# Kernel optimization log

Measured on AMD Instinct MI355X. Metric: run time of the kernel, lower is better.

The kernel has to match this reference:

```python
import jax, jax.numpy as jnp
import numpy as np


def setup_inputs() -> dict:
    key = jax.random.key(0)
    ks = jax.random.split(key, 7)
    B, EN, DE, E, U, T = 8, 512, 64, 512, 512, 100  # batch, max_words, max_label, emb, units, topics
    return {
        "en_seq": jax.random.normal(ks[0], (B, EN, E), dtype=jnp.float32),
        "de_seq": jax.random.normal(ks[1], (B, DE, E), dtype=jnp.float32),
        "topics": jax.random.uniform(ks[2], (B, T), dtype=jnp.float32),
        "w_en": jax.random.normal(ks[3], (E, U), dtype=jnp.float32) * 0.05,
        "w_de": jax.random.normal(ks[4], (E, U), dtype=jnp.float32) * 0.05,
        "nu": jax.random.normal(ks[5], (U,), dtype=jnp.float32) * 0.05,
        "wt": jax.random.normal(ks[6], (E, T), dtype=jnp.float32) * 0.05,
    }


def reference(en_seq, de_seq, topics, w_en, w_de, nu, wt):
    # Additive (Bahdanau-style) attention with a per-batch topic bias.
    att_en = jnp.einsum("bie,eu->biu", en_seq, w_en)        # [B, EN, U]
    att_de = jnp.einsum("bje,eu->bju", de_seq, w_de)        # [B, DE, U]
    topics_w = jnp.einsum("bt,ut->bu", topics, wt)          # [B, U] (wt is [E,U-dim? no: E==U])
    # co_m[b, j, i, u] = att_en[b,i,u] + att_de[b,j,u] + topics_w[b,u]
    co_m = jnp.tanh(att_en[:, None, :, :] + att_de[:, :, None, :]
                    + topics_w[:, None, None, :])           # [B, DE, EN, U]
    mu = jnp.einsum("bjiu,u->bji", co_m, nu)                # [B, DE, EN]
    alphas = jax.nn.softmax(mu, axis=-1)                    # softmax over encoder positions
    p_gen = jax.nn.sigmoid(mu)
    sum_en = jnp.einsum("bji,bie->bje", alphas, en_seq)     # attention-weighted encoder sum
    output = de_seq + sum_en
    return (output, alphas, p_gen)
```

## Files before the change

### kernel.cpp

```cpp
#include <hip/hip_runtime.h>
#include <hip/hip_bf16.h>

#define NB  8
#define ENW 512
#define DEW 64
#define EMB 512
#define UN  512
#define NT  100

#define KSCALE 2.8853900817779268f
#define L2E    1.4426950408889634f

typedef short bf16x8 __attribute__((ext_vector_type(8)));
typedef unsigned short u16x8 __attribute__((ext_vector_type(8)));
typedef float f32x4  __attribute__((ext_vector_type(4)));

__device__ __forceinline__ unsigned short f2bf(float f) {
    union { float f; unsigned int u; } v; v.f = f;
    unsigned int r = v.u + 0x7FFFu + ((v.u >> 16) & 1u);
    return (unsigned short)(r >> 16);
}

__device__ __forceinline__ float rlane(float v, int l) {
    return __int_as_float(__builtin_amdgcn_readlane(__float_as_int(v), l));
}

__global__ __launch_bounds__(256) void prep_kernel(const float* __restrict__ w_en,
                                                   const float* __restrict__ w_de,
                                                   const float* __restrict__ en,
                                                   const float* __restrict__ de,
                                                   const float* __restrict__ topics,
                                                   const float* __restrict__ wt_mat,
                                                   const float* __restrict__ nu,
                                                   unsigned short* __restrict__ wen_t,
                                                   unsigned short* __restrict__ wde_t,
                                                   unsigned short* __restrict__ en_bf,
                                                   unsigned short* __restrict__ de_bf,
                                                   float* __restrict__ tw2,
                                                   float* __restrict__ snu,
                                                   float* __restrict__ nu2) {
    const int bx = blockIdx.x, t = threadIdx.x;
    if (bx < 128) {
        __shared__ float tile[64][65];
        const float* w = (bx < 64) ? w_en : w_de;
        unsigned short* o = (bx < 64) ? wen_t : wde_t;
        const int tb = bx & 63;
        const int r0 = (tb >> 3) * 64;
        const int c0 = (tb & 7) * 64;
        const int rr = t >> 4, cc = (t & 15) * 4;
#pragma unroll
        for (int q = 0; q < 4; ++q) {
            float4 v = *(const float4*)(w + (size_t)(r0 + rr + 16 * q) * 512 + c0 + cc);
            *(float4*)&tile[rr + 16 * q][cc] = v;
        }
        __syncthreads();
#pragma unroll
        for (int q = 0; q < 4; ++q) {
            int ul = rr + 16 * q;
            int el = cc;
            ushort4 v;
            v.x = f2bf(KSCALE * tile[el][ul]);
            v.y = f2bf(KSCALE * tile[el + 1][ul]);
            v.z = f2bf(KSCALE * tile[el + 2][ul]);
            v.w = f2bf(KSCALE * tile[el + 3][ul]);
            *(ushort4*)(o + (size_t)(c0 + ul) * 512 + r0 + el) = v;
        }
    } else if (bx < 1280) {
        const bool is_en = (bx < 1152);
        const float* src = is_en ? en : de;
        unsigned short* dst = is_en ? en_bf : de_bf;
        const int idx = ((is_en ? (bx - 128) : (bx - 1152)) * 256 + t) * 8;
        float4 a0 = *(const float4*)(src + idx);
        float4 a1 = *(const float4*)(src + idx + 4);
        u16x8 o;
        o[0] = f2bf(a0.x); o[1] = f2bf(a0.y); o[2] = f2bf(a0.z); o[3] = f2bf(a0.w);
        o[4] = f2bf(a1.x); o[5] = f2bf(a1.y); o[6] = f2bf(a1.z); o[7] = f2bf(a1.w);
        *(u16x8*)(dst + idx) = o;
    } else if (bx < 1296) {
        int idx = (bx - 1280) * 256 + t;
        int b = idx >> 9, u = idx & 511;
        const float* tp = topics + b * NT;
        const float* wp = wt_mat + u * NT;
        float s = 0.f;
        for (int tt = 0; tt < NT; ++tt) s += tp[tt] * wp[tt];
        tw2[idx] = KSCALE * s;
    } else {
        __shared__ float red[256];
        float n0 = nu[t], n1 = nu[t + 256];
        nu2[t] = -2.f * n0;
        nu2[t + 256] = -2.f * n1;
        red[t] = n0 + n1;
        __syncthreads();
        for (int off = 128; off > 0; off >>= 1) {
            if (t < off) red[t] += red[t + off];
            __syncthreads();
        }
        if (t == 0) snu[0] = red[0];
    }
}

__global__ __launch_bounds__(256) void gemm_fused(const unsigned short* __restrict__ en_bf,
                                                  const unsigned short* __restrict__ de_bf,
                                                  const unsigned short* __restrict__ wen_t,
                                                  const unsigned short* __restrict__ wde_t,
                                                  const float* __restrict__ tw2,
                                                  float* __restrict__ Ea,
                                                  float* __restrict__ Eb) {
    const int K = 512, N = 512;
    const int bx = blockIdx.x;
    const bool is_de = (bx >= 64);
    const unsigned short* A = is_de ? de_bf : en_bf;
    const unsigned short* Bt = is_de ? wde_t : wen_t;
    float* C = is_de ? Eb : Ea;
    const int mb = is_de ? (bx - 64) : bx;

    const int lane = threadIdx.x & 63;
    const int wave = threadIdx.x >> 6;
    const int m0 = mb * 64 + wave * 16;
    const int n0 = blockIdx.y * 64;
    const int row = m0 + (lane & 15);
    const int kq  = (lane >> 4) * 8;

    f32x4 acc[4];
#pragma unroll
    for (int nn = 0; nn < 4; ++nn) acc[nn] = 0.f;

    const unsigned short* ap = A + (size_t)row * K + kq;
    const unsigned short* bp = Bt + (size_t)(n0 + (lane & 15)) * K + kq;
#pragma unroll 4
    for (int kc = 0; kc < K; kc += 32) {
        bf16x8 a = *(const bf16x8*)(ap + kc);
#pragma unroll
        for (int nn = 0; nn < 4; ++nn) {
            bf16x8 b = *(const bf16x8*)(bp + (size_t)nn * 16 * K + kc);
            acc[nn] = __builtin_amdgcn_mfma_f32_16x16x32_bf16(a, b, acc[nn], 0, 0, 0);
        }
    }
    const int crow = m0 + (lane >> 4) * 4;
    const int ccol = lane & 15;
#pragma unroll
    for (int nn = 0; nn < 4; ++nn)
#pragma unroll
        for (int r = 0; r < 4; ++r) {
            int rw = crow + r, cl = n0 + nn * 16 + ccol;
            float v = acc[nn][r];
            if (is_de) v += tw2[(rw >> 6) * 512 + cl];
            C[(size_t)rw * N + cl] = __builtin_amdgcn_exp2f(v);
        }
}

__global__ __launch_bounds__(256) void mu4_kernel(const float* __restrict__ Ea,
                                                  const float* __restrict__ Eb,
                                                  const float* __restrict__ nu2,
                                                  const float* __restrict__ snu,
                                                  float* __restrict__ mu) {
    __shared__ float As[16][132];
    __shared__ float Bs[16][132];
    __shared__ float Ns[128];
    const int t = threadIdx.x;
    const int bx = blockIdx.x;
    const int jg = bx & 3;
    const int isplit = (bx >> 2) & 31;
    const int b = bx >> 7;
    const int i0 = isplit * 16, j0 = jg * 16;
    const int il = t & 15, jr = t >> 4;

    const float* aeb = Ea + (size_t)(b * ENW + i0) * UN;
    const float* bib = Eb + (size_t)(b * DEW + j0) * UN;

    float s0 = 0.f, s1 = 0.f;
    for (int uc = 0; uc < 512; uc += 128) {
#pragma unroll
        for (int q = 0; q < 2; ++q) {
            int idx = q * 256 + t;
            int row = idx >> 5, c4 = idx & 31;
            float4 va = *(const float4*)(aeb + (size_t)row * UN + uc + c4 * 4);
            *(float4*)&As[row][c4 * 4] = va;
            float4 vb = *(const float4*)(bib + (size_t)row * UN + uc + c4 * 4);
            *(float4*)&Bs[row][c4 * 4] = vb;
        }
        if (t < 32) *(float4*)&Ns[t * 4] = *(const float4*)(nu2 + uc + t * 4);
        __syncthreads();
#pragma unroll 8
        for (int c = 0; c < 32; ++c) {
            float4 a  = *(const float4*)&As[il][c * 4];
            float4 bb = *(const float4*)&Bs[jr][c * 4];
            float4 nv = *(const float4*)&Ns[c * 4];
            float e0 = fmaf(a.x, bb.x, 1.f);
            float e1 = fmaf(a.y, bb.y, 1.f);
            float e2 = fmaf(a.z, bb.z, 1.f);
            float e3 = fmaf(a.w, bb.w, 1.f);
            s0 = fmaf(nv.x, __builtin_amdgcn_rcpf(e0), s0);
            s1 = fmaf(nv.y, __builtin_amdgcn_rcpf(e1), s1);
            s0 = fmaf(nv.z, __builtin_amdgcn_rcpf(e2), s0);
            s1 = fmaf(nv.w, __builtin_amdgcn_rcpf(e3), s1);
        }
        __syncthreads();
    }
    mu[(size_t)(b * DEW + j0 + jr) * ENW + i0 + il] = snu[0] + s0 + s1;
}

__global__ __launch_bounds__(256) void softfin_kernel(const float* __restrict__ mu,
                                                      const float* __restrict__ en,
                                                      const float* __restrict__ de,
                                                      float* __restrict__ out,
                                                      float* __restrict__ alphas,
                                                      float* __restrict__ p_gen) {
    __shared__ float Al[4][512];
    __shared__ float Ps[4][4][256];
    const int bx = blockIdx.x;
    const int eh = bx & 1;
    const int jq = (bx >> 1) & 15;
    const int b  = bx >> 5;
    const int t = threadIdx.x;
    const int wave = t >> 6, lane = t & 63;
    const int j0 = jq * 4;

    {
        const int bj = b * DEW + j0 + wave;
        const float* mup = mu + (size_t)bj * ENW;
        float v[8], a[8];
#pragma unroll
        for (int c = 0; c < 8; ++c) v[c] = mup[c * 64 + lane];
        float mx = v[0];
#pragma unroll
        for (int c = 1; c < 8; ++c) mx = fmaxf(mx, v[c]);
#pragma unroll
        for (int off = 32; off > 0; off >>= 1) mx = fmaxf(mx, __shfl_xor(mx, off));
        float s = 0.f;
#pragma unroll
        for (int c = 0; c < 8; ++c) { a[c] = __builtin_amdgcn_exp2f((v[c] - mx) * L2E); s += a[c]; }
#pragma unroll
        for (int off = 32; off > 0; off >>= 1) s += __shfl_xor(s, off);
        float inv = __builtin_amdgcn_rcpf(s);
#pragma unroll
        for (int c = 0; c < 8; ++c) {
            a[c] *= inv;
            Al[wave][c * 64 + lane] = a[c];
        }
        if (eh == 0) {
            float* alp = alphas + (size_t)bj * ENW;
            float* pgp = p_gen + (size_t)bj * ENW;
#pragma unroll
            for (int c = 0; c < 8; ++c) {
                alp[c * 64 + lane] = a[c];
                pgp[c * 64 + lane] = __builtin_amdgcn_rcpf(1.f + __builtin_amdgcn_exp2f(-v[c] * L2E));
            }
        }
    }
    __syncthreads();

    const int i0 = wave * 128;
    const float* enb = en + (size_t)b * ENW * EMB + eh * 256 + lane * 4;
    f32x4 acc[4];
#pragma unroll
    for (int jj = 0; jj < 4; ++jj) acc[jj] = 0.f;
    for (int ig = 0; ig < 128; ig += 4) {
        const int ib = i0 + ig;
        float4 al0 = *(const float4*)&Al[0][ib];
        float4 al1 = *(const float4*)&Al[1][ib];
        float4 al2 = *(const float4*)&Al[2][ib];
        float4 al3 = *(const float4*)&Al[3][ib];
#pragma unroll
        for (int r = 0; r < 4; ++r) {
            float4 x = *(const float4*)(enb + (size_t)(ib + r) * EMB);
            float w0 = (r == 0) ? al0.x : (r == 1) ? al0.y : (r == 2) ? al0.z : al0.w;
            float w1 = (r == 0) ? al1.x : (r == 1) ? al1.y : (r == 2) ? al1.z : al1.w;
            float w2 = (r == 0) ? al2.x : (r == 1) ? al2.y : (r == 2) ? al2.z : al2.w;
            float w3 = (r == 0) ? al3.x : (r == 1) ? al3.y : (r == 2) ? al3.z : al3.w;
            acc[0][0] = fmaf(w0, x.x, acc[0][0]); acc[0][1] = fmaf(w0, x.y, acc[0][1]);
            acc[0][2] = fmaf(w0, x.z, acc[0][2]); acc[0][3] = fmaf(w0, x.w, acc[0][3]);
            acc[1][0] = fmaf(w1, x.x, acc[1][0]); acc[1][1] = fmaf(w1, x.y, acc[1][1]);
            acc[1][2] = fmaf(w1, x.z, acc[1][2]); acc[1][3] = fmaf(w1, x.w, acc[1][3]);
            acc[2][0] = fmaf(w2, x.x, acc[2][0]); acc[2][1] = fmaf(w2, x.y, acc[2][1]);
            acc[2][2] = fmaf(w2, x.z, acc[2][2]); acc[2][3] = fmaf(w2, x.w, acc[2][3]);
            acc[3][0] = fmaf(w3, x.x, acc[3][0]); acc[3][1] = fmaf(w3, x.y, acc[3][1]);
            acc[3][2] = fmaf(w3, x.z, acc[3][2]); acc[3][3] = fmaf(w3, x.w, acc[3][3]);
        }
    }
#pragma unroll
    for (int jj = 0; jj < 4; ++jj)
        *(f32x4*)&Ps[wave][jj][lane * 4] = acc[jj];
    __syncthreads();

    {
        const int bj = b * DEW + j0 + wave;
        const int e = eh * 256 + lane * 4;
        float4 p0 = *(const float4*)&Ps[0][wave][lane * 4];
        float4 p1 = *(const float4*)&Ps[1][wave][lane * 4];
        float4 p2 = *(const float4*)&Ps[2][wave][lane * 4];
        float4 p3 = *(const float4*)&Ps[3][wave][lane * 4];
        float4 d = *(const float4*)(de + (size_t)bj * EMB + e);
        float4 o;
        o.x = d.x + (p0.x + p1.x) + (p2.x + p3.x);
        o.y = d.y + (p0.y + p1.y) + (p2.y + p3.y);
        o.z = d.z + (p0.z + p1.z) + (p2.z + p3.z);
        o.w = d.w + (p0.w + p1.w) + (p2.w + p3.w);
        *(float4*)(out + (size_t)bj * EMB + e) = o;
    }
}

extern "C" void kernel_launch(void* const* d_in, const int* in_sizes, int n_in,
                              void* d_out, int out_size, void* d_ws, size_t ws_size,
                              hipStream_t stream) {
    const float* en     = (const float*)d_in[0];
    const float* de     = (const float*)d_in[1];
    const float* topics = (const float*)d_in[2];
    const float* w_en   = (const float*)d_in[3];
    const float* w_de   = (const float*)d_in[4];
    const float* nu     = (const float*)d_in[5];
    const float* wt     = (const float*)d_in[6];

    float* out    = (float*)d_out;
    float* alphas = out + 262144;
    float* p_gen  = out + 524288;

    char* ws = (char*)d_ws;
    float* Ea             = (float*)(ws);
    float* Eb             = (float*)(ws + 8388608);
    float* tw2            = (float*)(ws + 9437184);
    float* mu             = (float*)(ws + 9453568);
    unsigned short* en_bf = (unsigned short*)(ws + 10502144);
    unsigned short* de_bf = (unsigned short*)(ws + 14696448);
    unsigned short* wen_t = (unsigned short*)(ws + 15220736);
    unsigned short* wde_t = (unsigned short*)(ws + 15745024);
    float* snu            = (float*)(ws + 16269312);
    float* nu2            = (float*)(ws + 16269328);

    prep_kernel<<<1297, 256, 0, stream>>>(w_en, w_de, en, de, topics, wt, nu,
                                          wen_t, wde_t, en_bf, de_bf, tw2, snu, nu2);
    gemm_fused<<<dim3(72, 8), 256, 0, stream>>>(en_bf, de_bf, wen_t, wde_t, tw2, Ea, Eb);
    mu4_kernel<<<1024, 256, 0, stream>>>(Ea, Eb, nu2, snu, mu);
    softfin_kernel<<<256, 256, 0, stream>>>(mu, en, de, out, alphas, p_gen);
}
```

Before: 141.4 us.

## Fuse activation bf16 conversion into GEMM and retile GEMM grid

Removes the separate pass that converts en/de activations to bf16 in the prep kernel; the GEMM now loads fp32 activations directly and converts them in registers with a cheaper rounding. The GEMM grid is retiled to 32x128 blocks over a 1D launch, and the mu kernel loads all of nu2 into shared memory once instead of per chunk. This saves a global write and re-read of the bf16 copies but doubles the A-operand bytes each GEMM wave loads, and the conversion is repeated per N-tile. The new rounding skips ties-to-even, which can change low-order bits.

```diff
diff --git a/kernel.cpp b/kernel.cpp
--- a/kernel.cpp
+++ b/kernel.cpp
@@ -12,7 +12,6 @@
 #define L2E    1.4426950408889634f
 
 typedef short bf16x8 __attribute__((ext_vector_type(8)));
-typedef unsigned short u16x8 __attribute__((ext_vector_type(8)));
 typedef float f32x4  __attribute__((ext_vector_type(4)));
 
 __device__ __forceinline__ unsigned short f2bf(float f) {
@@ -21,21 +20,18 @@
     return (unsigned short)(r >> 16);
 }
 
-__device__ __forceinline__ float rlane(float v, int l) {
-    return __int_as_float(__builtin_amdgcn_readlane(__float_as_int(v), l));
+__device__ __forceinline__ unsigned short f2bf_fast(float f) {
+    union { float f; unsigned int u; } v; v.f = f;
+    return (unsigned short)((v.u + 0x8000u) >> 16);
 }
 
 __global__ __launch_bounds__(256) void prep_kernel(const float* __restrict__ w_en,
                                                    const float* __restrict__ w_de,
-                                                   const float* __restrict__ en,
-                                                   const float* __restrict__ de,
                                                    const float* __restrict__ topics,
                                                    const float* __restrict__ wt_mat,
                                                    const float* __restrict__ nu,
                                                    unsigned short* __restrict__ wen_t,
                                                    unsigned short* __restrict__ wde_t,
-                                                   unsigned short* __restrict__ en_bf,
-                                                   unsigned short* __restrict__ de_bf,
                                                    float* __restrict__ tw2,
                                                    float* __restrict__ snu,
                                                    float* __restrict__ nu2) {
@@ -65,19 +61,8 @@
             v.w = f2bf(KSCALE * tile[el + 3][ul]);
             *(ushort4*)(o + (size_t)(c0 + ul) * 512 + r0 + el) = v;
         }
-    } else if (bx < 1280) {
-        const bool is_en = (bx < 1152);
-        const float* src = is_en ? en : de;
-        unsigned short* dst = is_en ? en_bf : de_bf;
-        const int idx = ((is_en ? (bx - 128) : (bx - 1152)) * 256 + t) * 8;
-        float4 a0 = *(const float4*)(src + idx);
-        float4 a1 = *(const float4*)(src + idx + 4);
-        u16x8 o;
-        o[0] = f2bf(a0.x); o[1] = f2bf(a0.y); o[2] = f2bf(a0.z); o[3] = f2bf(a0.w);
-        o[4] = f2bf(a1.x); o[5] = f2bf(a1.y); o[6] = f2bf(a1.z); o[7] = f2bf(a1.w);
-        *(u16x8*)(dst + idx) = o;
-    } else if (bx < 1296) {
-        int idx = (bx - 1280) * 256 + t;
+    } else if (bx < 144) {
+        int idx = (bx - 128) * 256 + t;
         int b = idx >> 9, u = idx & 511;
         const float* tp = topics + b * NT;
         const float* wp = wt_mat + u * NT;
@@ -99,25 +84,26 @@
     }
 }
 
-__global__ __launch_bounds__(256) void gemm_fused(const unsigned short* __restrict__ en_bf,
-                                                  const unsigned short* __restrict__ de_bf,
-                                                  const unsigned short* __restrict__ wen_t,
-                                                  const unsigned short* __restrict__ wde_t,
-                                                  const float* __restrict__ tw2,
-                                                  float* __restrict__ Ea,
-                                                  float* __restrict__ Eb) {
+__global__ __launch_bounds__(256) void gemm_v2(const float* __restrict__ en,
+                                               const float* __restrict__ de,
+                                               const unsigned short* __restrict__ wen_t,
+                                               const unsigned short* __restrict__ wde_t,
+                                               const float* __restrict__ tw2,
+                                               float* __restrict__ Ea,
+                                               float* __restrict__ Eb) {
     const int K = 512, N = 512;
     const int bx = blockIdx.x;
-    const bool is_de = (bx >= 64);
-    const unsigned short* A = is_de ? de_bf : en_bf;
+    const bool is_de = (bx >= 512);
+    const float* A = is_de ? de : en;
     const unsigned short* Bt = is_de ? wde_t : wen_t;
     float* C = is_de ? Eb : Ea;
-    const int mb = is_de ? (bx - 64) : bx;
+    const int bb = is_de ? (bx - 512) : bx;
+    const int mb = bb >> 2, nq = bb & 3;
 
     const int lane = threadIdx.x & 63;
     const int wave = threadIdx.x >> 6;
-    const int m0 = mb * 64 + wave * 16;
-    const int n0 = blockIdx.y * 64;
+    const int m0 = mb * 32 + (wave & 1) * 16;
+    const int n0 = nq * 128 + (wave >> 1) * 64;
     const int row = m0 + (lane & 15);
     const int kq  = (lane >> 4) * 8;
 
@@ -125,11 +111,17 @@
 #pragma unroll
     for (int nn = 0; nn < 4; ++nn) acc[nn] = 0.f;
 
-    const unsigned short* ap = A + (size_t)row * K + kq;
+    const float* ap = A + (size_t)row * K + kq;
     const unsigned short* bp = Bt + (size_t)(n0 + (lane & 15)) * K + kq;
 #pragma unroll 4
     for (int kc = 0; kc < K; kc += 32) {
-        bf16x8 a = *(const bf16x8*)(ap + kc);
+        float4 a0 = *(const float4*)(ap + kc);
+        float4 a1 = *(const float4*)(ap + kc + 4);
+        bf16x8 a;
+        a[0] = (short)f2bf_fast(a0.x); a[1] = (short)f2bf_fast(a0.y);
+        a[2] = (short)f2bf_fast(a0.z); a[3] = (short)f2bf_fast(a0.w);
+        a[4] = (short)f2bf_fast(a1.x); a[5] = (short)f2bf_fast(a1.y);
+        a[6] = (short)f2bf_fast(a1.z); a[7] = (short)f2bf_fast(a1.w);
 #pragma unroll
         for (int nn = 0; nn < 4; ++nn) {
             bf16x8 b = *(const bf16x8*)(bp + (size_t)nn * 16 * K + kc);
@@ -156,7 +148,7 @@
                                                   float* __restrict__ mu) {
     __shared__ float As[16][132];
     __shared__ float Bs[16][132];
-    __shared__ float Ns[128];
+    __shared__ float Ns[512];
     const int t = threadIdx.x;
     const int bx = blockIdx.x;
     const int jg = bx & 3;
@@ -165,6 +157,9 @@
     const int i0 = isplit * 16, j0 = jg * 16;
     const int il = t & 15, jr = t >> 4;
 
+    Ns[t] = nu2[t];
+    Ns[t + 256] = nu2[t + 256];
+
     const float* aeb = Ea + (size_t)(b * ENW + i0) * UN;
     const float* bib = Eb + (size_t)(b * DEW + j0) * UN;
 
@@ -179,13 +174,12 @@
             float4 vb = *(const float4*)(bib + (size_t)row * UN + uc + c4 * 4);
             *(float4*)&Bs[row][c4 * 4] = vb;
         }
-        if (t < 32) *(float4*)&Ns[t * 4] = *(const float4*)(nu2 + uc + t * 4);
         __syncthreads();
 #pragma unroll 8
         for (int c = 0; c < 32; ++c) {
             float4 a  = *(const float4*)&As[il][c * 4];
             float4 bb = *(const float4*)&Bs[jr][c * 4];
-            float4 nv = *(const float4*)&Ns[c * 4];
+            float4 nv = *(const float4*)&Ns[uc + c * 4];
             float e0 = fmaf(a.x, bb.x, 1.f);
             float e1 = fmaf(a.y, bb.y, 1.f);
             float e2 = fmaf(a.z, bb.z, 1.f);
@@ -320,16 +314,14 @@
     float* Eb             = (float*)(ws + 8388608);
     float* tw2            = (float*)(ws + 9437184);
     float* mu             = (float*)(ws + 9453568);
-    unsigned short* en_bf = (unsigned short*)(ws + 10502144);
-    unsigned short* de_bf = (unsigned short*)(ws + 14696448);
-    unsigned short* wen_t = (unsigned short*)(ws + 15220736);
-    unsigned short* wde_t = (unsigned short*)(ws + 15745024);
-    float* snu            = (float*)(ws + 16269312);
-    float* nu2            = (float*)(ws + 16269328);
-
-    prep_kernel<<<1297, 256, 0, stream>>>(w_en, w_de, en, de, topics, wt, nu,
-                                          wen_t, wde_t, en_bf, de_bf, tw2, snu, nu2);
-    gemm_fused<<<dim3(72, 8), 256, 0, stream>>>(en_bf, de_bf, wen_t, wde_t, tw2, Ea, Eb);
+    unsigned short* wen_t = (unsigned short*)(ws + 10502144);
+    unsigned short* wde_t = (unsigned short*)(ws + 11026432);
+    float* snu            = (float*)(ws + 11550720);
+    float* nu2            = (float*)(ws + 11550736);
+
+    prep_kernel<<<145, 256, 0, stream>>>(w_en, w_de, topics, wt, nu,
+                                         wen_t, wde_t, tw2, snu, nu2);
+    gemm_v2<<<576, 256, 0, stream>>>(en, de, wen_t, wde_t, tw2, Ea, Eb);
     mu4_kernel<<<1024, 256, 0, stream>>>(Ea, Eb, nu2, snu, mu);
     softfin_kernel<<<256, 256, 0, stream>>>(mu, en, de, out, alphas, p_gen);
 }
```

Measured after the change: 144.3 us. 2.0% more time.
